# Optimization experiments

Measured on AMD Instinct MI355X. Metric: run time of the kernel, lower is better.

## Reference

```python
import itertools
import jax, jax.numpy as jnp
import numpy as np

B, N_TOK, C = 256, 196, 512
NUM_HEADS, KEY_DIM, ATTN_RATIO, RESOLUTION = 8, 32, 4.0, 14
D_V = int(ATTN_RATIO * KEY_DIM)        # 128
DH = D_V * NUM_HEADS                   # 1024
H_QKV = DH + 2 * KEY_DIM * NUM_HEADS   # 1536
SCALE = KEY_DIM ** (-0.5)


def _build_bias_idxs(resolution):
    points = list(itertools.product(range(resolution), range(resolution)))
    attention_offsets = {}
    idxs = []
    for p1 in points:
        for p2 in points:
            offset = (abs(p1[0] - p2[0]), abs(p1[1] - p2[1]))
            if offset not in attention_offsets:
                attention_offsets[offset] = len(attention_offsets)
            idxs.append(attention_offsets[offset])
    n = len(points)
    return np.array(idxs, dtype=np.int64).reshape(n, n), len(attention_offsets)


def setup_inputs() -> dict:
    key = jax.random.key(0)
    ks = jax.random.split(key, 6)
    idxs_np, n_offsets = _build_bias_idxs(RESOLUTION)  # (196,196), 196 offsets
    return {
        "x": jax.random.normal(ks[0], (B, N_TOK, C), dtype=jnp.float32),
        "qkv_w": jax.random.normal(ks[1], (H_QKV, C), dtype=jnp.float32) * (C ** -0.5),
        "qkv_b": jax.random.normal(ks[2], (H_QKV,), dtype=jnp.float32) * 0.01,
        "proj_w": jax.random.normal(ks[3], (C, DH), dtype=jnp.float32) * (DH ** -0.5),
        "proj_b": jax.random.normal(ks[4], (C,), dtype=jnp.float32) * 0.01,
        "attention_biases": jax.random.normal(ks[5], (NUM_HEADS, n_offsets), dtype=jnp.float32) * 0.02,
        "bias_idxs": jnp.asarray(idxs_np),
    }


def reference(x, qkv_w, qkv_b, proj_w, proj_b, attention_biases, bias_idxs):
    Bsz, N, _ = x.shape
    # qkv projection: (B, N, H_QKV) -> (B, heads, N, 2*key_dim + d_v)
    qkv = x @ qkv_w.T + qkv_b
    qkv = qkv.reshape(Bsz, N, NUM_HEADS, -1).transpose(0, 2, 1, 3)
    q = qkv[..., :KEY_DIM]
    k = qkv[..., KEY_DIM:2 * KEY_DIM]
    v = qkv[..., 2 * KEY_DIM:]
    # learned relative-position bias gather: (heads, N, N)
    bias = attention_biases[:, bias_idxs]
    attn = jnp.einsum("bhnd,bhmd->bhnm", q, k) * SCALE + bias
    attn = jax.nn.softmax(attn, axis=-1)
    out = jnp.einsum("bhnm,bhmd->bhnd", attn, v)  # (B, heads, N, d_v)
    out = out.transpose(0, 2, 1, 3).reshape(Bsz, N, DH)
    return out @ proj_w.T + proj_b
```

## Files before the change

kernel.cpp:

```cpp
#include <hip/hip_runtime.h>

typedef __attribute__((ext_vector_type(8))) short bf16x8;
typedef __attribute__((ext_vector_type(4))) float f32x4;
typedef unsigned short u16;
typedef unsigned int   u32;

#define NTOK  196
#define NH    8
#define DVDIM 128
#define CDIM  512
#define DH    1024
#define SCALE2 0.25505654708103197f
#define NEG_BIG -1.0e30f
#define LOG2E 1.4426950408889634f
#define VSTRIDE 200
#define RESCALE_THR 8.0f

__device__ __forceinline__ u16 f2bf(float f) {
  u32 u = __builtin_bit_cast(u32, f);
  u32 r = u + 0x7FFFu + ((u >> 16) & 1u);
  return (u16)(r >> 16);
}

__device__ __forceinline__ u32 cvtpk(float lo, float hi) {
  u32 r;
  asm("v_cvt_pk_bf16_f32 %0, %1, %2" : "=v"(r) : "v"(lo), "v"(hi));
  return r;
}

__device__ __forceinline__ void stage16(const void* g, char* lds_wave_base, int lane) {
#if __has_builtin(__builtin_amdgcn_global_load_lds)
  __builtin_amdgcn_global_load_lds(
      (const __attribute__((address_space(1))) unsigned int*)g,
      (__attribute__((address_space(3))) unsigned int*)lds_wave_base, 16, 0, 0);
#else
  *(uint4*)(lds_wave_base + lane * 16) = *(const uint4*)g;
#endif
}

__global__ __launch_bounds__(256)
void cvt_k(const float* __restrict__ s, u16* __restrict__ d, int n8) {
  int i = blockIdx.x * 256 + threadIdx.x;
  if (i < n8) {
    const float4* sp = (const float4*)s + (size_t)i * 2;
    float4 a = sp[0], b = sp[1];
    uint4 o;
    o.x = (u32)f2bf(a.x) | ((u32)f2bf(a.y) << 16);
    o.y = (u32)f2bf(a.z) | ((u32)f2bf(a.w) << 16);
    o.z = (u32)f2bf(b.x) | ((u32)f2bf(b.y) << 16);
    o.w = (u32)f2bf(b.z) | ((u32)f2bf(b.w) << 16);
    ((uint4*)d)[i] = o;
  }
}

__global__ __launch_bounds__(224)
void biasT_k(const float* __restrict__ ab, const int* __restrict__ bidx,
             float* __restrict__ bT) {
  const int m = threadIdx.x, j = blockIdx.x, h = blockIdx.y;
  float v = NEG_BIG;
  if (j < NTOK && m < NTOK) v = ab[h * NTOK + bidx[m * NTOK + j]] * LOG2E;
  bT[((size_t)h * 256 + j) * 224 + m] = v;
}

template<int K, int NB, int EPI>
__global__ __launch_bounds__(256)
void gemm_k(const u16* __restrict__ A, const u16* __restrict__ W,
            const float* __restrict__ bias,
            u16* __restrict__ q, u16* __restrict__ kk, u16* __restrict__ vT,
            float* __restrict__ out)
{
  __shared__ __align__(16) u16 As[128 * 32];
  __shared__ __align__(16) u16 Bs[128 * 32];
  const int tid  = threadIdx.x;
  const int bid  = blockIdx.x;
  const int xcd  = bid & 7, t = bid >> 3;
  const int bn   = t % NB, bm = xcd * 49 + t / NB;
  const int lane = tid & 63, w = tid >> 6;
  const int c16  = lane & 15, quad = lane >> 4;
  const int wm   = (w >> 1) * 64, wn = (w & 1) * 64;
  f32x4 acc[4][4] = {};

  const u16* Ab = A + (size_t)bm * 128 * K;
  const u16* Wb = W + (size_t)bn * 128 * K;
  char* ldsA = (char*)As + w * 1024;
  char* ldsB = (char*)Bs + w * 1024;

  for (int k0 = 0; k0 < K; k0 += 32) {
    #pragma unroll
    for (int p = 0; p < 2; ++p) {
      const int i = p * 256 + tid;
      const int m = i >> 2, kp = (i & 3) * 8;
      stage16(Ab + (size_t)m * K + k0 + kp, ldsA + p * 4096, lane);
      stage16(Wb + (size_t)m * K + k0 + kp, ldsB + p * 4096, lane);
    }
    __syncthreads();
    bf16x8 af[4], bfr[4];
    #pragma unroll
    for (int mi = 0; mi < 4; ++mi)
      af[mi] = *(const bf16x8*)&As[(wm + mi * 16 + c16) * 32 + quad * 8];
    #pragma unroll
    for (int ni = 0; ni < 4; ++ni)
      bfr[ni] = *(const bf16x8*)&Bs[(wn + ni * 16 + c16) * 32 + quad * 8];
    #pragma unroll
    for (int mi = 0; mi < 4; ++mi)
      #pragma unroll
      for (int ni = 0; ni < 4; ++ni)
        acc[mi][ni] = __builtin_amdgcn_mfma_f32_16x16x32_bf16(af[mi], bfr[ni], acc[mi][ni], 0, 0, 0);
    __syncthreads();
  }

  if (EPI == 0) {
    #pragma unroll
    for (int ni = 0; ni < 4; ++ni) {
      const int gn = bn * 128 + wn + ni * 16 + c16;
      const int h = gn / 192, d = gn - h * 192;
      const float bv = bias[gn];
      #pragma unroll
      for (int mi = 0; mi < 4; ++mi) {
        const int gm0 = bm * 128 + wm + mi * 16 + quad * 4;
        const int bb = gm0 / 196, tok0 = gm0 - bb * 196;
        const size_t bhh = (size_t)bb * 8 + h;
        const float v0 = acc[mi][ni][0] + bv, v1 = acc[mi][ni][1] + bv;
        const float v2 = acc[mi][ni][2] + bv, v3 = acc[mi][ni][3] + bv;
        if (d < 64) {
          u16* dst = (d < 32) ? (q  + (bhh * 196 + tok0) * 32 + d)
                              : (kk + (bhh * 196 + tok0) * 32 + (d - 32));
          dst[0] = f2bf(v0); dst[32] = f2bf(v1); dst[64] = f2bf(v2); dst[96] = f2bf(v3);
        } else {
          ushort4 pk = { f2bf(v0), f2bf(v1), f2bf(v2), f2bf(v3) };
          *(ushort4*)&vT[(bhh * 128 + (d - 64)) * VSTRIDE + tok0] = pk;
        }
      }
    }
  } else {
    #pragma unroll
    for (int ni = 0; ni < 4; ++ni) {
      const int gn = bn * 128 + wn + ni * 16 + c16;
      const float bv = bias[gn];
      #pragma unroll
      for (int mi = 0; mi < 4; ++mi) {
        const int gm0 = bm * 128 + wm + mi * 16 + quad * 4;
        #pragma unroll
        for (int r = 0; r < 4; ++r)
          out[(size_t)(gm0 + r) * CDIM + gn] = acc[mi][ni][r] + bv;
      }
    }
  }
}

__global__ __launch_bounds__(256)
void attn_k(const u16* __restrict__ q, const u16* __restrict__ kk,
            const u16* __restrict__ vT, const float* __restrict__ bT,
            u16* __restrict__ Ob)
{
  __shared__ __align__(16) u16 k_s[64 * 40];
  __shared__ __align__(16) u16 vt_s[128 * 72];
  __shared__ __align__(16) u16 p_s[4 * 16 * 72];

  const int bh = blockIdx.x;
  const int b = bh >> 3, h = bh & 7;
  const int tid = threadIdx.x;
  const int lane = tid & 63, w = tid >> 6;
  const int c16 = lane & 15, quad = lane >> 4;
  const u16* qb = q  + (size_t)bh * (NTOK * 32);
  const u16* kb = kk + (size_t)bh * (NTOK * 32);
  const u16* vb = vT + (size_t)bh * (DVDIM * VSTRIDE);
  const float* bTh = bT + (size_t)h * 256 * 224;

  const int ti  = blockIdx.y * 4 + w;
  const bool act = (ti < 13);
  const int tok = min(ti * 16 + c16, NTOK - 1);
  const bf16x8 qf = *(const bf16x8*)(qb + (size_t)tok * 32 + quad * 8);
  float mx = NEG_BIG, lsum = 0.f;
  f32x4 oacc[8] = {};
  const f32x4 zf = {0.f, 0.f, 0.f, 0.f};
  u16* pw = p_s + w * 16 * 72;

  for (int kc = 0; kc < 4; ++kc) {
    {
      const int key = min(kc * 64 + (tid >> 2), NTOK - 1);
      const int part = (tid & 3) * 8;
      *(uint4*)&k_s[(tid >> 2) * 40 + part] = *(const uint4*)(kb + (size_t)key * 32 + part);
    }
    #pragma unroll
    for (int it = 0; it < 4; ++it) {
      const int idx = tid + it * 256;
      const int dv = idx >> 3, kp = (idx & 7) * 8;
      const int col = min(kc * 64 + kp, 192);
      *(uint4*)&vt_s[dv * 72 + kp] = *(const uint4*)(vb + (size_t)dv * VSTRIDE + col);
    }
    __syncthreads();

    if (act) {
      f32x4 sc[4];
      __builtin_amdgcn_s_setprio(1);
      #pragma unroll
      for (int nt = 0; nt < 4; ++nt) {
        bf16x8 kf = *(const bf16x8*)&k_s[(nt * 16 + c16) * 40 + quad * 8];
        sc[nt] = __builtin_amdgcn_mfma_f32_16x16x32_bf16(kf, qf, zf, 0, 0, 0);
      }
      __builtin_amdgcn_s_setprio(0);

      const int qg = min(ti * 16 + c16, 223);
      float ntmx[4];
      #pragma unroll
      for (int nt = 0; nt < 4; ++nt) {
        const float* bp = bTh + (size_t)(kc * 64 + nt * 16 + quad * 4) * 224 + qg;
        #pragma unroll
        for (int r = 0; r < 4; ++r)
          sc[nt][r] = sc[nt][r] * SCALE2 + bp[r * 224];
        ntmx[nt] = fmaxf(fmaxf(sc[nt][0], sc[nt][1]), fmaxf(sc[nt][2], sc[nt][3]));
      }
      const float cmx = fmaxf(fmaxf(ntmx[0], ntmx[1]), fmaxf(ntmx[2], ntmx[3]));

      float alpha = 1.0f;
      if (__ballot(cmx > mx + RESCALE_THR)) {
        float rmx = fmaxf(cmx, __shfl_xor(cmx, 16));
        rmx = fmaxf(rmx, __shfl_xor(rmx, 32));
        const float nmx = fmaxf(mx, rmx);
        alpha = exp2f(mx - nmx);
        mx = nmx;
        float a4[4];
        #pragma unroll
        for (int r = 0; r < 4; ++r) a4[r] = __shfl(alpha, quad * 4 + r);
        #pragma unroll
        for (int nt = 0; nt < 8; ++nt)
          #pragma unroll
          for (int r = 0; r < 4; ++r) oacc[nt][r] *= a4[r];
      }

      const float m = mx;
      float csum = 0.f;
      #pragma unroll
      for (int nt = 0; nt < 4; ++nt) {
        const float p0 = exp2f(sc[nt][0] - m), p1 = exp2f(sc[nt][1] - m);
        const float p2 = exp2f(sc[nt][2] - m), p3 = exp2f(sc[nt][3] - m);
        csum += (p0 + p1) + (p2 + p3);
        uint2 pk;
        pk.x = cvtpk(p0, p1);
        pk.y = cvtpk(p2, p3);
        *(uint2*)&pw[c16 * 72 + nt * 16 + quad * 4] = pk;
      }
      csum += __shfl_xor(csum, 16);
      csum += __shfl_xor(csum, 32);
      lsum = lsum * alpha + csum;

      __builtin_amdgcn_s_setprio(1);
      #pragma unroll
      for (int ks = 0; ks < 2; ++ks) {
        bf16x8 ap = *(const bf16x8*)&pw[c16 * 72 + ks * 32 + quad * 8];
        #pragma unroll
        for (int nt = 0; nt < 8; ++nt) {
          bf16x8 bv = *(const bf16x8*)&vt_s[(nt * 16 + c16) * 72 + ks * 32 + quad * 8];
          oacc[nt] = __builtin_amdgcn_mfma_f32_16x16x32_bf16(ap, bv, oacc[nt], 0, 0, 0);
        }
      }
      __builtin_amdgcn_s_setprio(0);
    }
    __syncthreads();
  }

  if (act) {
    float lr[4];
    #pragma unroll
    for (int r = 0; r < 4; ++r) lr[r] = __shfl(lsum, quad * 4 + r);
    #pragma unroll
    for (int r = 0; r < 4; ++r) {
      const int m = ti * 16 + quad * 4 + r;
      if (m < NTOK) {
        const float inv = 1.0f / lr[r];
        #pragma unroll
        for (int nt = 0; nt < 8; ++nt)
          Ob[((size_t)b * NTOK + m) * DH + h * DVDIM + nt * 16 + c16] =
              f2bf(oacc[nt][r] * inv);
      }
    }
  }
}

extern "C" void kernel_launch(void* const* d_in, const int* in_sizes, int n_in,
                              void* d_out, int out_size, void* d_ws, size_t ws_size,
                              hipStream_t stream) {
  const float* x      = (const float*)d_in[0];
  const float* qkv_w  = (const float*)d_in[1];
  const float* qkv_b  = (const float*)d_in[2];
  const float* proj_w = (const float*)d_in[3];
  const float* proj_b = (const float*)d_in[4];
  const float* ab     = (const float*)d_in[5];
  const int*   bidx   = (const int*)d_in[6];
  float* out = (float*)d_out;

  char* p = (char*)d_ws;
  u16*   qw  = (u16*)(p);
  u16*   kw  = (u16*)(p + 25690112);
  u16*   vTw = (u16*)(p + 51380224);
  u16*   w1b = (u16*)(p + 156237824);
  u16*   w3b = (u16*)(p + 157810688);
  float* bT  = (float*)(p + 158859264);
  u16*   xb  = (u16*)(p + 160694272);
  u16*   Ob  = (u16*)(p + 160694272);

  cvt_k<<<12544, 256, 0, stream>>>(x,      xb,  3211264);
  cvt_k<<<  384, 256, 0, stream>>>(qkv_w,  w1b,   98304);
  cvt_k<<<  256, 256, 0, stream>>>(proj_w, w3b,   65536);
  biasT_k<<<dim3(256, 8), 224, 0, stream>>>(ab, bidx, bT);

  gemm_k<512, 12, 0><<<4704, 256, 0, stream>>>(xb, w1b, qkv_b, qw, kw, vTw, nullptr);

  attn_k<<<dim3(2048, 4), 256, 0, stream>>>(qw, kw, vTw, bT, Ob);

  gemm_k<1024, 4, 1><<<1568, 256, 0, stream>>>(Ob, w3b, proj_b, nullptr, nullptr, nullptr, out);
}
```

Before: 540.5 us.

## Load full K/V per head into LDS once and loop query tiles per block

The attention kernel now uses one block per (batch, head) instead of four. It stages the entire K and V^T for that head into a single large LDS buffer (about 80 KB), using what appears to be a direct-to-LDS staging helper for V, and zeroes the padded V columns. Each wave then loops over its query tiles with no per-chunk __syncthreads, and the 13th tile is given to a rotating wave. This removes the fourfold redundant K/V loads and the per-chunk barriers, at the cost of high LDS usage per block, which lowers occupancy, and an uneven split of tiles across waves.

```diff
diff --git a/kernel.cpp b/kernel.cpp
--- a/kernel.cpp
+++ b/kernel.cpp
@@ -153,9 +153,10 @@
             const u16* __restrict__ vT, const float* __restrict__ bT,
             u16* __restrict__ Ob)
 {
-  __shared__ __align__(16) u16 k_s[64 * 40];
-  __shared__ __align__(16) u16 vt_s[128 * 72];
-  __shared__ __align__(16) u16 p_s[4 * 16 * 72];
+  __shared__ __align__(16) char smem[80896];
+  u16* k_lds  = (u16*)smem;
+  u16* vt_lds = (u16*)(smem + 20480);
+  u16* p_lds  = (u16*)(smem + 71680);
 
   const int bh = blockIdx.x;
   const int b = bh >> 3, h = bh & 7;
@@ -166,42 +167,47 @@
   const u16* kb = kk + (size_t)bh * (NTOK * 32);
   const u16* vb = vT + (size_t)bh * (DVDIM * VSTRIDE);
   const float* bTh = bT + (size_t)h * 256 * 224;
-
-  const int ti  = blockIdx.y * 4 + w;
-  const bool act = (ti < 13);
-  const int tok = min(ti * 16 + c16, NTOK - 1);
-  const bf16x8 qf = *(const bf16x8*)(qb + (size_t)tok * 32 + quad * 8);
-  float mx = NEG_BIG, lsum = 0.f;
-  f32x4 oacc[8] = {};
   const f32x4 zf = {0.f, 0.f, 0.f, 0.f};
-  u16* pw = p_s + w * 16 * 72;
-
-  for (int kc = 0; kc < 4; ++kc) {
-    {
-      const int key = min(kc * 64 + (tid >> 2), NTOK - 1);
-      const int part = (tid & 3) * 8;
-      *(uint4*)&k_s[(tid >> 2) * 40 + part] = *(const uint4*)(kb + (size_t)key * 32 + part);
-    }
-    #pragma unroll
-    for (int it = 0; it < 4; ++it) {
-      const int idx = tid + it * 256;
-      const int dv = idx >> 3, kp = (idx & 7) * 8;
-      const int col = min(kc * 64 + kp, 192);
-      *(uint4*)&vt_s[dv * 72 + kp] = *(const uint4*)(vb + (size_t)dv * VSTRIDE + col);
-    }
-    __syncthreads();
-
-    if (act) {
+  u16* pw = p_lds + w * 16 * 72;
+
+  {
+    const char* vbb = (const char*)vb;
+    for (int c = w; c < 50; c += 4)
+      stage16(vbb + c * 1024 + lane * 16, (char*)vt_lds + c * 1024, lane);
+  }
+  #pragma unroll
+  for (int p = 0; p < 4; ++p) {
+    const int i = p * 256 + tid;
+    const int row = i >> 2, part = (i & 3) * 8;
+    const uint4 val = *(const uint4*)(kb + (size_t)min(row, NTOK - 1) * 32 + part);
+    *(uint4*)&k_lds[row * 40 + part] = val;
+  }
+  __syncthreads();
+  {
+    const int row = tid >> 1, half = tid & 1;
+    *(u32*)&vt_lds[row * VSTRIDE + 196 + half * 2] = 0u;
+  }
+  __syncthreads();
+
+  const int nt_iter = 3 + ((w == (bh & 3)) ? 1 : 0);
+  for (int t = 0; t < nt_iter; ++t) {
+    const int ti = (t < 3) ? (w + 4 * t) : 12;
+    const int tok = min(ti * 16 + c16, NTOK - 1);
+    const bf16x8 qf = *(const bf16x8*)(qb + (size_t)tok * 32 + quad * 8);
+    const int qg = min(ti * 16 + c16, 223);
+    float mx = NEG_BIG, lsum = 0.f;
+    f32x4 oacc[8] = {};
+
+    for (int kc = 0; kc < 4; ++kc) {
       f32x4 sc[4];
       __builtin_amdgcn_s_setprio(1);
       #pragma unroll
       for (int nt = 0; nt < 4; ++nt) {
-        bf16x8 kf = *(const bf16x8*)&k_s[(nt * 16 + c16) * 40 + quad * 8];
+        bf16x8 kf = *(const bf16x8*)&k_lds[(kc * 64 + nt * 16 + c16) * 40 + quad * 8];
         sc[nt] = __builtin_amdgcn_mfma_f32_16x16x32_bf16(kf, qf, zf, 0, 0, 0);
       }
       __builtin_amdgcn_s_setprio(0);
 
-      const int qg = min(ti * 16 + c16, 223);
       float ntmx[4];
       #pragma unroll
       for (int nt = 0; nt < 4; ++nt) {
@@ -251,16 +257,13 @@
         bf16x8 ap = *(const bf16x8*)&pw[c16 * 72 + ks * 32 + quad * 8];
         #pragma unroll
         for (int nt = 0; nt < 8; ++nt) {
-          bf16x8 bv = *(const bf16x8*)&vt_s[(nt * 16 + c16) * 72 + ks * 32 + quad * 8];
+          bf16x8 bv = *(const bf16x8*)&vt_lds[(nt * 16 + c16) * VSTRIDE + kc * 64 + ks * 32 + quad * 8];
           oacc[nt] = __builtin_amdgcn_mfma_f32_16x16x32_bf16(ap, bv, oacc[nt], 0, 0, 0);
         }
       }
       __builtin_amdgcn_s_setprio(0);
     }
-    __syncthreads();
-  }
-
-  if (act) {
+
     float lr[4];
     #pragma unroll
     for (int r = 0; r < 4; ++r) lr[r] = __shfl(lsum, quad * 4 + r);
@@ -307,7 +310,7 @@
 
   gemm_k<512, 12, 0><<<4704, 256, 0, stream>>>(xb, w1b, qkv_b, qw, kw, vTw, nullptr);
 
-  attn_k<<<dim3(2048, 4), 256, 0, stream>>>(qw, kw, vTw, bT, Ob);
+  attn_k<<<2048, 256, 0, stream>>>(qw, kw, vTw, bT, Ob);
 
   gemm_k<1024, 4, 1><<<1568, 256, 0, stream>>>(Ob, w3b, proj_b, nullptr, nullptr, nullptr, out);
 }
```

Result: no change. 541.6 us (+0.2%).
